# Performance work log

Hardware: AMD Instinct MI355X
Metric: run time of the kernel (lower is better)

## Reference

```python
import jax, jax.numpy as jnp
import numpy as np

N_SRC = 50000
N_DST = 50000
IN_FEATS = 256
OUT_FEATS = 32
NUM_HEADS = 4
N_EDGES = 800000


def setup_inputs() -> dict:
    key = jax.random.key(0)
    ks = jax.random.split(key, 7)
    h_src = jax.random.normal(ks[0], (N_SRC, IN_FEATS), dtype=jnp.float32)
    h_dst = jax.random.normal(ks[1], (N_DST, IN_FEATS), dtype=jnp.float32)
    # xavier-normal-ish scaling for the shared fc weight
    W = jax.random.normal(ks[2], (IN_FEATS, NUM_HEADS * OUT_FEATS), dtype=jnp.float32) * (
        jnp.sqrt(2.0) * jnp.sqrt(2.0 / (IN_FEATS + NUM_HEADS * OUT_FEATS))
    )
    attn_l = jax.random.normal(ks[3], (NUM_HEADS, OUT_FEATS), dtype=jnp.float32) * 0.1
    attn_r = jax.random.normal(ks[4], (NUM_HEADS, OUT_FEATS), dtype=jnp.float32) * 0.1
    src_idx = jax.random.randint(ks[5], (N_EDGES,), 0, N_SRC, dtype=jnp.int32)
    dst_idx = jax.random.randint(ks[6], (N_EDGES,), 0, N_DST, dtype=jnp.int32)
    return {"h_src": h_src, "h_dst": h_dst, "W": W, "attn_l": attn_l,
            "attn_r": attn_r, "src_idx": src_idx, "dst_idx": dst_idx}


def reference(h_src, h_dst, W, attn_l, attn_r, src_idx, dst_idx):
    H, F = NUM_HEADS, OUT_FEATS
    # shared linear projection (no bias), reshape to [N, H, F]
    ft_src = (h_src @ W).reshape(-1, H, F)            # [N_src, H, F]
    ft_dst = (h_dst @ W).reshape(-1, H, F)            # [N_dst, H, F]
    # per-node attention logits, [N, H]
    el = jnp.einsum('nhf,hf->nh', ft_src, attn_l)
    er = jnp.einsum('nhf,hf->nh', ft_dst, attn_r)
    # u_add_v gather over edges, LeakyReLU(0.2) -> [E, H]
    e = jax.nn.leaky_relu(el[src_idx] + er[dst_idx], negative_slope=0.2)
    # edge softmax over incoming edges of each destination node
    smax = jax.ops.segment_max(e, dst_idx, num_segments=N_DST)   # [N_dst, H]
    e_exp = jnp.exp(e - smax[dst_idx])                           # [E, H]
    ssum = jax.ops.segment_sum(e_exp, dst_idx, num_segments=N_DST)
    a = e_exp / ssum[dst_idx]                                    # [E, H]
    # u_mul_e + scatter-sum aggregation -> [N_dst, H, F]
    msg = ft_src[src_idx] * a[:, :, None]
    rst = jax.ops.segment_sum(msg, dst_idx, num_segments=N_DST)
    return rst
```

## Files before the change

### kernel.cpp

```cpp
#include <hip/hip_runtime.h>

#define IN_FEATS 256
#define OUT_FEATS 32
#define NUM_HEADS 4
#define NHF 128

#define NCH 512

typedef __attribute__((ext_vector_type(8))) short short8;
typedef __attribute__((ext_vector_type(4))) float f32x4;

__device__ inline unsigned short f2bf(float f) {
    unsigned int u = __builtin_bit_cast(unsigned int, f);
    u = (u + 0x7fff + ((u >> 16) & 1)) >> 16;
    return (unsigned short)u;
}
__device__ inline float bfhi2f(unsigned int packed_hi) {
    return __builtin_bit_cast(float, packed_hi);
}

__global__ __launch_bounds__(256) void prep_hist(const float* __restrict__ W,
                                                 const float* __restrict__ attn_r,
                                                 const int* __restrict__ dst,
                                                 float* __restrict__ v,
                                                 unsigned short* __restrict__ Wt,
                                                 int* __restrict__ partial,
                                                 int E) {
    const int t = threadIdx.x;
    const int b = blockIdx.x;
    if (b < 128) {
        Wt[b * 256 + t] = f2bf(W[(size_t)t * NHF + b]);
    } else if (b == 128) {
        for (int p = t; p < IN_FEATS * NUM_HEADS; p += 256) {
            int k = p >> 2, h = p & 3;
            const float* wr = W + (size_t)k * NHF + h * OUT_FEATS;
            const float* ar = attn_r + h * OUT_FEATS;
            float s = 0.f;
            #pragma unroll
            for (int f = 0; f < OUT_FEATS; ++f) s += wr[f] * ar[f];
            v[p] = s;
        }
    } else {
        __shared__ int cnt[256];
        const int hb = b - 129;
        const int chunk = (E + NCH - 1) / NCH;
        const int e0 = hb * chunk;
        const int e1 = min(e0 + chunk, E);
        cnt[t] = 0;
        __syncthreads();
        for (int e = e0 + t; e < e1; e += 256)
            atomicAdd(&cnt[dst[e] >> 8], 1);
        __syncthreads();
        partial[hb * 256 + t] = cnt[t];
    }
}

__global__ __launch_bounds__(256) void bin_pairs(const int* __restrict__ src,
                                                 const int* __restrict__ dst,
                                                 const int* __restrict__ partial,
                                                 unsigned int* __restrict__ pairs,
                                                 int* __restrict__ bbase,
                                                 int E) {
    __shared__ int sc[256];
    __shared__ int basel[256];
    __shared__ int cnt[256];
    const int t = threadIdx.x;
    const int b = blockIdx.x;
    const int chunk = (E + NCH - 1) / NCH;
    const int e0 = b * chunk;
    const int e1 = min(e0 + chunk, E);

    int dreg[7], sreg[7];
    #pragma unroll
    for (int i = 0; i < 7; ++i) {
        const int e = e0 + t + i * 256;
        const bool ok = e < e1;
        dreg[i] = ok ? dst[e] : 0;
        sreg[i] = ok ? src[e] : 0;
    }

    int colsum = 0, rowpref = 0;
    {
        int bb = 0;
        #pragma unroll 8
        for (; bb < b; ++bb) {
            const int pv = partial[bb * 256 + t];
            colsum += pv;
            rowpref += pv;
        }
        #pragma unroll 8
        for (; bb < NCH; ++bb) colsum += partial[bb * 256 + t];
    }
    sc[t] = colsum;
    __syncthreads();
    #pragma unroll
    for (int d = 1; d < 256; d <<= 1) {
        int x = (t >= d) ? sc[t - d] : 0;
        __syncthreads();
        sc[t] += x;
        __syncthreads();
    }
    if (b == 0) {
        bbase[t] = sc[t] - colsum;
        if (t == 255) bbase[256] = sc[255];
    }
    basel[t] = (sc[t] - colsum) + rowpref;
    cnt[t] = 0;
    __syncthreads();

    #pragma unroll
    for (int i = 0; i < 7; ++i) {
        const int e = e0 + t + i * 256;
        if (e < e1) {
            const int d = dreg[i];
            const int bk = d >> 8;
            const int o = atomicAdd(&cnt[bk], 1);
            pairs[basel[bk] + o] = (unsigned int)sreg[i] | ((unsigned int)(d & 255) << 16);
        }
    }
    for (int e = e0 + t + 7 * 256; e < e1; e += 256) {
        const int d = dst[e];
        const int bk = d >> 8;
        const int o = atomicAdd(&cnt[bk], 1);
        pairs[basel[bk] + o] = (unsigned int)src[e] | ((unsigned int)(d & 255) << 16);
    }
}

__global__ __launch_bounds__(256) void er_fine(const float* __restrict__ hdst,
                                               const float* __restrict__ v,
                                               float* __restrict__ er, int M,
                                               const unsigned int* __restrict__ pairs,
                                               const int* __restrict__ bbase,
                                               int* __restrict__ off,
                                               int* __restrict__ csr_src,
                                               int nb, int n_dst, int E) {
    __shared__ int cnt[256];
    __shared__ int cur[256];

    if (blockIdx.x < (unsigned)nb) {
        const int t = threadIdx.x;
        const int b = blockIdx.x;
        const int p0 = bbase[b], p1 = bbase[b + 1];
        cnt[t] = 0;
        __syncthreads();
        for (int p = p0 + t; p < p1; p += 256)
            atomicAdd(&cnt[pairs[p] >> 16], 1);
        __syncthreads();
        int vv = cnt[t];
        cur[t] = vv;
        __syncthreads();
        #pragma unroll
        for (int d = 1; d < 256; d <<= 1) {
            int x = (t >= d) ? cur[t - d] : 0;
            __syncthreads();
            cur[t] += x;
            __syncthreads();
        }
        int ex = cur[t] - vv;
        int node = b * 256 + t;
        if (node < n_dst) off[node] = p0 + ex;
        if (b == 0 && t == 0) off[n_dst] = E;
        __syncthreads();
        cur[t] = ex;
        __syncthreads();
        for (int p = p0 + t; p < p1; p += 256) {
            unsigned int pr = pairs[p];
            int o = atomicAdd(&cur[pr >> 16], 1);
            csr_src[p0 + o] = (int)(pr & 0xffffu);
        }
        return;
    }

    int wid  = ((blockIdx.x - nb) * 256 + threadIdx.x) >> 6;
    int lane = threadIdx.x & 63;
    if (wid >= M) return;
    const float4 x = *(const float4*)(hdst + (size_t)wid * IN_FEATS + lane * 4);
    const float4* vp = (const float4*)(v + (size_t)lane * 16);
    float4 v0 = vp[0], v1 = vp[1], v2 = vp[2], v3 = vp[3];
    float a0 = x.x * v0.x + x.y * v1.x + x.z * v2.x + x.w * v3.x;
    float a1 = x.x * v0.y + x.y * v1.y + x.z * v2.y + x.w * v3.y;
    float a2 = x.x * v0.z + x.y * v1.z + x.z * v2.z + x.w * v3.z;
    float a3 = x.x * v0.w + x.y * v1.w + x.z * v2.w + x.w * v3.w;
    #pragma unroll
    for (int m = 32; m >= 1; m >>= 1) {
        a0 += __shfl_xor(a0, m, 64);
        a1 += __shfl_xor(a1, m, 64);
        a2 += __shfl_xor(a2, m, 64);
        a3 += __shfl_xor(a3, m, 64);
    }
    if (lane == 0) *(float4*)(er + (size_t)wid * 4) = make_float4(a0, a1, a2, a3);
}

#define BSTRIDE 136
__global__ __launch_bounds__(256) void gemm_el(const float* __restrict__ A,
                                               const unsigned short* __restrict__ Wt,
                                               const float* __restrict__ attn_l,
                                               unsigned short* __restrict__ ft16,
                                               float* __restrict__ el, int M) {
    __shared__ unsigned short WtL[128 * 256];

    const int wave = threadIdx.x >> 6;
    const int lane = threadIdx.x & 63;
    const int quad = lane >> 4;
    const int mc   = lane & 15;
    const int row_base = blockIdx.x * 64 + wave * 16;

    for (int i = threadIdx.x; i < 4096; i += 256) {
        const int n = i >> 5, c = i & 31;
        const int cs = (c + n) & 31;
        *(uint4*)(WtL + n * 256 + cs * 8) = *(const uint4*)(Wt + n * 256 + c * 8);
    }

    float al[8];
    #pragma unroll
    for (int t = 0; t < 8; ++t) al[t] = attn_l[(t >> 1) * 32 + (t & 1) * 16 + mc];

    const int rowA = min(row_base + mc, M - 1);
    const float* arow = A + (size_t)rowA * IN_FEATS;

    float4 a[8][2];
    #pragma unroll
    for (int kk = 0; kk < 8; ++kk) {
        a[kk][0] = *(const float4*)(arow + kk * 32 + quad * 8);
        a[kk][1] = *(const float4*)(arow + kk * 32 + quad * 8 + 4);
    }

    f32x4 acc[8];
    #pragma unroll
    for (int t = 0; t < 8; ++t) acc[t] = (f32x4){0.f, 0.f, 0.f, 0.f};

    __syncthreads();

    #pragma unroll
    for (int kk = 0; kk < 8; ++kk) {
        short8 af;
        af[0] = (short)f2bf(a[kk][0].x); af[1] = (short)f2bf(a[kk][0].y);
        af[2] = (short)f2bf(a[kk][0].z); af[3] = (short)f2bf(a[kk][0].w);
        af[4] = (short)f2bf(a[kk][1].x); af[5] = (short)f2bf(a[kk][1].y);
        af[6] = (short)f2bf(a[kk][1].z); af[7] = (short)f2bf(a[kk][1].w);
        #pragma unroll
        for (int t = 0; t < 8; ++t) {
            const int n = t * 16 + mc;
            const int c = ((kk << 2) + quad + n) & 31;
            const short8 bf = *(const short8*)(WtL + n * 256 + c * 8);
            acc[t] = __builtin_amdgcn_mfma_f32_16x16x32_bf16(af, bf, acc[t], 0, 0, 0);
        }
    }

    float elp[4][4];
    #pragma unroll
    for (int v = 0; v < 4; ++v)
        #pragma unroll
        for (int h = 0; h < 4; ++h) elp[v][h] = 0.f;
    #pragma unroll
    for (int v = 0; v < 4; ++v)
        #pragma unroll
        for (int t = 0; t < 8; ++t) elp[v][t >> 1] += acc[t][v] * al[t];
    #pragma unroll
    for (int v = 0; v < 4; ++v)
        #pragma unroll
        for (int h = 0; h < 4; ++h) {
            #pragma unroll
            for (int d = 1; d < 16; d <<= 1)
                elp[v][h] += __shfl_xor(elp[v][h], d, 64);
        }

    #pragma unroll
    for (int v = 0; v < 4; ++v) {
        const int rg = row_base + quad * 4 + v;
        if (rg < M && mc < 4) {
            float ev = (mc == 0) ? elp[v][0] : (mc == 1) ? elp[v][1]
                     : (mc == 2) ? elp[v][2] : elp[v][3];
            el[(size_t)rg * 4 + mc] = ev;
        }
    }

    __syncthreads();
    #pragma unroll
    for (int v = 0; v < 4; ++v) {
        const int lr = wave * 16 + quad * 4 + v;
        #pragma unroll
        for (int t = 0; t < 8; ++t)
            WtL[lr * BSTRIDE + t * 16 + mc] = f2bf(acc[t][v]);
    }
    __syncthreads();
    const int rows_in_blk = min(64, M - blockIdx.x * 64);
    for (int i = threadIdx.x; i < 64 * 16; i += 256) {
        const int lr = i >> 4, seg = i & 15;
        if (lr < rows_in_blk)
            *(uint4*)(ft16 + (size_t)(blockIdx.x * 64 + lr) * NHF + seg * 8) =
                *(const uint4*)(WtL + lr * BSTRIDE + seg * 8);
    }
}

__global__ __launch_bounds__(256) void agg_pull(const int* __restrict__ off,
                                                const int* __restrict__ csr_src,
                                                const float* __restrict__ el,
                                                const float* __restrict__ er,
                                                const uint2* __restrict__ ftp,
                                                float* __restrict__ out, int n_dst) {
    const int wid  = (blockIdx.x * blockDim.x + threadIdx.x) >> 6;
    const int lane = threadIdx.x & 63;
    const int half = lane >> 5;
    const int hl   = lane & 31;
    const int node = wid * 2 + half;
    const bool valid = node < n_dst;
    const int nc = valid ? node : 0;
    const int h  = hl >> 3;
    const float er_h = er[nc * 4 + h];
    const int start = off[nc];
    const int end   = valid ? off[nc + 1] : start;
    const int deg   = end - start;
    const int last  = max(end - 1, 0);

    const int sl = csr_src[min(start + hl, last)];

    const int mdeg  = max(deg, __shfl_xor(deg, 32, 64));
    const int iters = (min(mdeg, 32) + 7) >> 3;

    float a0 = 0.f, a1 = 0.f, a2 = 0.f, a3 = 0.f, sw = 0.f;

    float e[8]; uint2 q[8];
    #pragma unroll
    for (int j = 0; j < 8; ++j) {
        const int s = __shfl(sl, j, 32);
        e[j] = el[s * 4 + h];
        q[j] = ftp[s * 32 + hl];
    }

    for (int i = 0; i < iters; ++i) {
        float f[8]; uint2 r[8];
        const int jn = (i + 1) << 3;
        #pragma unroll
        for (int j = 0; j < 8; ++j) {
            const int s = __shfl(sl, min(jn + j, 31), 32);
            f[j] = el[s * 4 + h];
            r[j] = ftp[s * 32 + hl];
        }

        const int kb = start + (i << 3);
        #pragma unroll
        for (int j = 0; j < 8; ++j) {
            float x = e[j] + er_h;
            x = fmaxf(x, 0.2f * x);
            const float w = (kb + j < end) ? __expf(x) : 0.f;
            sw += w;
            a0 = fmaf(bfhi2f(q[j].x << 16),          w, a0);
            a1 = fmaf(bfhi2f(q[j].x & 0xffff0000u),  w, a1);
            a2 = fmaf(bfhi2f(q[j].y << 16),          w, a2);
            a3 = fmaf(bfhi2f(q[j].y & 0xffff0000u),  w, a3);
        }

        #pragma unroll
        for (int j = 0; j < 8; ++j) { e[j] = f[j]; q[j] = r[j]; }
    }

    for (int k = start + 32; k < end; ++k) {
        const int s = csr_src[k];
        float x = el[s * 4 + h] + er_h;
        x = fmaxf(x, 0.2f * x);
        const float w = __expf(x);
        const uint2 qq = ftp[s * 32 + hl];
        sw += w;
        a0 = fmaf(bfhi2f(qq.x << 16),         w, a0);
        a1 = fmaf(bfhi2f(qq.x & 0xffff0000u), w, a1);
        a2 = fmaf(bfhi2f(qq.y << 16),         w, a2);
        a3 = fmaf(bfhi2f(qq.y & 0xffff0000u), w, a3);
    }

    if (valid) {
        const float inv = (deg > 0) ? 1.f / sw : 0.f;
        float4 r;
        r.x = a0 * inv; r.y = a1 * inv; r.z = a2 * inv; r.w = a3 * inv;
        *(float4*)(out + (size_t)node * NHF + hl * 4) = r;
    }
}

extern "C" void kernel_launch(void* const* d_in, const int* in_sizes, int n_in,
                              void* d_out, int out_size, void* d_ws, size_t ws_size,
                              hipStream_t stream) {
    const float* h_src  = (const float*)d_in[0];
    const float* h_dst  = (const float*)d_in[1];
    const float* W      = (const float*)d_in[2];
    const float* attn_l = (const float*)d_in[3];
    const float* attn_r = (const float*)d_in[4];
    const int* src_idx  = (const int*)d_in[5];
    const int* dst_idx  = (const int*)d_in[6];

    const int n_src = in_sizes[0] / IN_FEATS;
    const int n_dst = in_sizes[1] / IN_FEATS;
    const int E     = in_sizes[5];

    const int nb = (n_dst + 255) >> 8;

    char* ws = (char*)d_ws;
    size_t o = 0;
    float* v       = (float*)(ws + o); o += 4096;
    float* el      = (float*)(ws + o); o += (size_t)n_src * 4 * sizeof(float);
    float* er      = (float*)(ws + o); o += (size_t)n_dst * 4 * sizeof(float);
    int*   off     = (int*)(ws + o);   o += ((size_t)n_dst + 16) * sizeof(int);
    int*   bbase   = (int*)(ws + o);   o += 260 * sizeof(int);
    int*   partial = (int*)(ws + o);   o += (size_t)NCH * 256 * sizeof(int);
    unsigned short* Wt = (unsigned short*)(ws + o); o += (size_t)NHF * IN_FEATS * sizeof(unsigned short);
    int*   csr_src = (int*)(ws + o);   o += (size_t)E * sizeof(int);
    unsigned int* pairs = (unsigned int*)(ws + o); o += (size_t)E * sizeof(unsigned int);
    unsigned short* ft16 = (unsigned short*)(ws + o); o += (size_t)n_src * NHF * sizeof(unsigned short);

    float* out = (float*)d_out;

    prep_hist<<<129 + NCH, 256, 0, stream>>>(W, attn_r, dst_idx, v, Wt, partial, E);
    bin_pairs<<<NCH, 256, 0, stream>>>(src_idx, dst_idx, partial, pairs, bbase, E);
    gemm_el<<<(n_src + 63) / 64, 256, 0, stream>>>(h_src, Wt, attn_l, ft16, el, n_src);
    {
        const int er_blocks = (n_dst * 64 + 255) / 256;
        er_fine<<<nb + er_blocks, 256, 0, stream>>>(h_dst, v, er, n_dst, pairs,
                                                    bbase, off, csr_src, nb, n_dst, E);
    }
    {
        const int nwave = (n_dst + 1) >> 1;
        agg_pull<<<(nwave + 3) / 4, 256, 0, stream>>>(off, csr_src, el, er,
                                                      (const uint2*)ft16, out, n_dst);
    }
}
```

Before: 234.9 us.

## Merge edge binning and GEMM into one launch; store CSR sources as 16-bit

The bin_pairs and gemm_el kernels become one launch, with the first NCH blocks doing edge binning and the rest doing the bf16 MFMA projection, so the two independent stages overlap and one launch is saved. CSR source indices are now stored as unsigned short instead of int, halving that array's write and read traffic in er_fine and agg_pull. The binning blocks now reserve the GEMM's 64KB shared buffer, which can lower their occupancy. The 16-bit index depends on n_src fitting in 16 bits, which the existing pair packing already assumed.

```diff
diff --git a/kernel.cpp b/kernel.cpp
--- a/kernel.cpp
+++ b/kernel.cpp
@@ -55,74 +55,179 @@
     }
 }
 
-__global__ __launch_bounds__(256) void bin_pairs(const int* __restrict__ src,
-                                                 const int* __restrict__ dst,
-                                                 const int* __restrict__ partial,
-                                                 unsigned int* __restrict__ pairs,
-                                                 int* __restrict__ bbase,
-                                                 int E) {
-    __shared__ int sc[256];
-    __shared__ int basel[256];
-    __shared__ int cnt[256];
-    const int t = threadIdx.x;
-    const int b = blockIdx.x;
-    const int chunk = (E + NCH - 1) / NCH;
-    const int e0 = b * chunk;
-    const int e1 = min(e0 + chunk, E);
-
-    int dreg[7], sreg[7];
-    #pragma unroll
-    for (int i = 0; i < 7; ++i) {
-        const int e = e0 + t + i * 256;
-        const bool ok = e < e1;
-        dreg[i] = ok ? dst[e] : 0;
-        sreg[i] = ok ? src[e] : 0;
-    }
-
-    int colsum = 0, rowpref = 0;
-    {
-        int bb = 0;
-        #pragma unroll 8
-        for (; bb < b; ++bb) {
-            const int pv = partial[bb * 256 + t];
-            colsum += pv;
-            rowpref += pv;
-        }
-        #pragma unroll 8
-        for (; bb < NCH; ++bb) colsum += partial[bb * 256 + t];
-    }
-    sc[t] = colsum;
-    __syncthreads();
-    #pragma unroll
-    for (int d = 1; d < 256; d <<= 1) {
-        int x = (t >= d) ? sc[t - d] : 0;
-        __syncthreads();
-        sc[t] += x;
-        __syncthreads();
-    }
-    if (b == 0) {
-        bbase[t] = sc[t] - colsum;
-        if (t == 255) bbase[256] = sc[255];
-    }
-    basel[t] = (sc[t] - colsum) + rowpref;
-    cnt[t] = 0;
-    __syncthreads();
-
-    #pragma unroll
-    for (int i = 0; i < 7; ++i) {
-        const int e = e0 + t + i * 256;
-        if (e < e1) {
-            const int d = dreg[i];
+#define BSTRIDE 136
+__global__ __launch_bounds__(256) void bin_gemm(const int* __restrict__ src,
+                                                const int* __restrict__ dst,
+                                                const int* __restrict__ partial,
+                                                unsigned int* __restrict__ pairs,
+                                                int* __restrict__ bbase,
+                                                int E,
+                                                const float* __restrict__ A,
+                                                const unsigned short* __restrict__ Wt,
+                                                const float* __restrict__ attn_l,
+                                                unsigned short* __restrict__ ft16,
+                                                float* __restrict__ el, int M) {
+    __shared__ unsigned short WtL[128 * 256];
+
+    if (blockIdx.x < NCH) {
+        int* sc    = (int*)WtL;
+        int* basel = (int*)WtL + 256;
+        int* cnt   = (int*)WtL + 512;
+        const int t = threadIdx.x;
+        const int b = blockIdx.x;
+        const int chunk = (E + NCH - 1) / NCH;
+        const int e0 = b * chunk;
+        const int e1 = min(e0 + chunk, E);
+
+        int dreg[7], sreg[7];
+        #pragma unroll
+        for (int i = 0; i < 7; ++i) {
+            const int e = e0 + t + i * 256;
+            const bool ok = e < e1;
+            dreg[i] = ok ? dst[e] : 0;
+            sreg[i] = ok ? src[e] : 0;
+        }
+
+        int colsum = 0, rowpref = 0;
+        {
+            int bb = 0;
+            #pragma unroll 8
+            for (; bb < b; ++bb) {
+                const int pv = partial[bb * 256 + t];
+                colsum += pv;
+                rowpref += pv;
+            }
+            #pragma unroll 8
+            for (; bb < NCH; ++bb) colsum += partial[bb * 256 + t];
+        }
+        sc[t] = colsum;
+        __syncthreads();
+        #pragma unroll
+        for (int d = 1; d < 256; d <<= 1) {
+            int x = (t >= d) ? sc[t - d] : 0;
+            __syncthreads();
+            sc[t] += x;
+            __syncthreads();
+        }
+        if (b == 0) {
+            bbase[t] = sc[t] - colsum;
+            if (t == 255) bbase[256] = sc[255];
+        }
+        basel[t] = (sc[t] - colsum) + rowpref;
+        cnt[t] = 0;
+        __syncthreads();
+
+        #pragma unroll
+        for (int i = 0; i < 7; ++i) {
+            const int e = e0 + t + i * 256;
+            if (e < e1) {
+                const int d = dreg[i];
+                const int bk = d >> 8;
+                const int o = atomicAdd(&cnt[bk], 1);
+                pairs[basel[bk] + o] = (unsigned int)sreg[i] | ((unsigned int)(d & 255) << 16);
+            }
+        }
+        for (int e = e0 + t + 7 * 256; e < e1; e += 256) {
+            const int d = dst[e];
             const int bk = d >> 8;
             const int o = atomicAdd(&cnt[bk], 1);
-            pairs[basel[bk] + o] = (unsigned int)sreg[i] | ((unsigned int)(d & 255) << 16);
-        }
-    }
-    for (int e = e0 + t + 7 * 256; e < e1; e += 256) {
-        const int d = dst[e];
-        const int bk = d >> 8;
-        const int o = atomicAdd(&cnt[bk], 1);
-        pairs[basel[bk] + o] = (unsigned int)src[e] | ((unsigned int)(d & 255) << 16);
+            pairs[basel[bk] + o] = (unsigned int)src[e] | ((unsigned int)(d & 255) << 16);
+        }
+        return;
+    }
+
+    const int gb   = blockIdx.x - NCH;
+    const int wave = threadIdx.x >> 6;
+    const int lane = threadIdx.x & 63;
+    const int quad = lane >> 4;
+    const int mc   = lane & 15;
+    const int row_base = gb * 64 + wave * 16;
+
+    for (int i = threadIdx.x; i < 4096; i += 256) {
+        const int n = i >> 5, c = i & 31;
+        const int cs = (c + n) & 31;
+        *(uint4*)(WtL + n * 256 + cs * 8) = *(const uint4*)(Wt + n * 256 + c * 8);
+    }
+
+    float al[8];
+    #pragma unroll
+    for (int t = 0; t < 8; ++t) al[t] = attn_l[(t >> 1) * 32 + (t & 1) * 16 + mc];
+
+    const int rowA = min(row_base + mc, M - 1);
+    const float* arow = A + (size_t)rowA * IN_FEATS;
+
+    float4 a[8][2];
+    #pragma unroll
+    for (int kk = 0; kk < 8; ++kk) {
+        a[kk][0] = *(const float4*)(arow + kk * 32 + quad * 8);
+        a[kk][1] = *(const float4*)(arow + kk * 32 + quad * 8 + 4);
+    }
+
+    f32x4 acc[8];
+    #pragma unroll
+    for (int t = 0; t < 8; ++t) acc[t] = (f32x4){0.f, 0.f, 0.f, 0.f};
+
+    __syncthreads();
+
+    #pragma unroll
+    for (int kk = 0; kk < 8; ++kk) {
+        short8 af;
+        af[0] = (short)f2bf(a[kk][0].x); af[1] = (short)f2bf(a[kk][0].y);
+        af[2] = (short)f2bf(a[kk][0].z); af[3] = (short)f2bf(a[kk][0].w);
+        af[4] = (short)f2bf(a[kk][1].x); af[5] = (short)f2bf(a[kk][1].y);
+        af[6] = (short)f2bf(a[kk][1].z); af[7] = (short)f2bf(a[kk][1].w);
+        #pragma unroll
+        for (int t = 0; t < 8; ++t) {
+            const int n = t * 16 + mc;
+            const int c = ((kk << 2) + quad + n) & 31;
+            const short8 bf = *(const short8*)(WtL + n * 256 + c * 8);
+            acc[t] = __builtin_amdgcn_mfma_f32_16x16x32_bf16(af, bf, acc[t], 0, 0, 0);
+        }
+    }
+
+    float elp[4][4];
+    #pragma unroll
+    for (int v = 0; v < 4; ++v)
+        #pragma unroll
+        for (int h = 0; h < 4; ++h) elp[v][h] = 0.f;
+    #pragma unroll
+    for (int v = 0; v < 4; ++v)
+        #pragma unroll
+        for (int t = 0; t < 8; ++t) elp[v][t >> 1] += acc[t][v] * al[t];
+    #pragma unroll
+    for (int v = 0; v < 4; ++v)
+        #pragma unroll
+        for (int h = 0; h < 4; ++h) {
+            #pragma unroll
+            for (int d = 1; d < 16; d <<= 1)
+                elp[v][h] += __shfl_xor(elp[v][h], d, 64);
+        }
+
+    #pragma unroll
+    for (int v = 0; v < 4; ++v) {
+        const int rg = row_base + quad * 4 + v;
+        if (rg < M && mc < 4) {
+            float ev = (mc == 0) ? elp[v][0] : (mc == 1) ? elp[v][1]
+                     : (mc == 2) ? elp[v][2] : elp[v][3];
+            el[(size_t)rg * 4 + mc] = ev;
+        }
+    }
+
+    __syncthreads();
+    #pragma unroll
+    for (int v = 0; v < 4; ++v) {
+        const int lr = wave * 16 + quad * 4 + v;
+        #pragma unroll
+        for (int t = 0; t < 8; ++t)
+            WtL[lr * BSTRIDE + t * 16 + mc] = f2bf(acc[t][v]);
+    }
+    __syncthreads();
+    const int rows_in_blk = min(64, M - gb * 64);
+    for (int i = threadIdx.x; i < 64 * 16; i += 256) {
+        const int lr = i >> 4, seg = i & 15;
+        if (lr < rows_in_blk)
+            *(uint4*)(ft16 + (size_t)(gb * 64 + lr) * NHF + seg * 8) =
+                *(const uint4*)(WtL + lr * BSTRIDE + seg * 8);
     }
 }
 
@@ -132,7 +237,7 @@
                                                const unsigned int* __restrict__ pairs,
                                                const int* __restrict__ bbase,
                                                int* __restrict__ off,
-                                               int* __restrict__ csr_src,
+                                               unsigned short* __restrict__ csr16,
                                                int nb, int n_dst, int E) {
     __shared__ int cnt[256];
     __shared__ int cur[256];
@@ -166,7 +271,7 @@
         for (int p = p0 + t; p < p1; p += 256) {
             unsigned int pr = pairs[p];
             int o = atomicAdd(&cur[pr >> 16], 1);
-            csr_src[p0 + o] = (int)(pr & 0xffffu);
+            csr16[p0 + o] = (unsigned short)(pr & 0xffffu);
         }
         return;
     }
@@ -191,110 +296,8 @@
     if (lane == 0) *(float4*)(er + (size_t)wid * 4) = make_float4(a0, a1, a2, a3);
 }
 
-#define BSTRIDE 136
-__global__ __launch_bounds__(256) void gemm_el(const float* __restrict__ A,
-                                               const unsigned short* __restrict__ Wt,
-                                               const float* __restrict__ attn_l,
-                                               unsigned short* __restrict__ ft16,
-                                               float* __restrict__ el, int M) {
-    __shared__ unsigned short WtL[128 * 256];
-
-    const int wave = threadIdx.x >> 6;
-    const int lane = threadIdx.x & 63;
-    const int quad = lane >> 4;
-    const int mc   = lane & 15;
-    const int row_base = blockIdx.x * 64 + wave * 16;
-
-    for (int i = threadIdx.x; i < 4096; i += 256) {
-        const int n = i >> 5, c = i & 31;
-        const int cs = (c + n) & 31;
-        *(uint4*)(WtL + n * 256 + cs * 8) = *(const uint4*)(Wt + n * 256 + c * 8);
-    }
-
-    float al[8];
-    #pragma unroll
-    for (int t = 0; t < 8; ++t) al[t] = attn_l[(t >> 1) * 32 + (t & 1) * 16 + mc];
-
-    const int rowA = min(row_base + mc, M - 1);
-    const float* arow = A + (size_t)rowA * IN_FEATS;
-
-    float4 a[8][2];
-    #pragma unroll
-    for (int kk = 0; kk < 8; ++kk) {
-        a[kk][0] = *(const float4*)(arow + kk * 32 + quad * 8);
-        a[kk][1] = *(const float4*)(arow + kk * 32 + quad * 8 + 4);
-    }
-
-    f32x4 acc[8];
-    #pragma unroll
-    for (int t = 0; t < 8; ++t) acc[t] = (f32x4){0.f, 0.f, 0.f, 0.f};
-
-    __syncthreads();
-
-    #pragma unroll
-    for (int kk = 0; kk < 8; ++kk) {
-        short8 af;
-        af[0] = (short)f2bf(a[kk][0].x); af[1] = (short)f2bf(a[kk][0].y);
-        af[2] = (short)f2bf(a[kk][0].z); af[3] = (short)f2bf(a[kk][0].w);
-        af[4] = (short)f2bf(a[kk][1].x); af[5] = (short)f2bf(a[kk][1].y);
-        af[6] = (short)f2bf(a[kk][1].z); af[7] = (short)f2bf(a[kk][1].w);
-        #pragma unroll
-        for (int t = 0; t < 8; ++t) {
-            const int n = t * 16 + mc;
-            const int c = ((kk << 2) + quad + n) & 31;
-            const short8 bf = *(const short8*)(WtL + n * 256 + c * 8);
-            acc[t] = __builtin_amdgcn_mfma_f32_16x16x32_bf16(af, bf, acc[t], 0, 0, 0);
-        }
-    }
-
-    float elp[4][4];
-    #pragma unroll
-    for (int v = 0; v < 4; ++v)
-        #pragma unroll
-        for (int h = 0; h < 4; ++h) elp[v][h] = 0.f;
-    #pragma unroll
-    for (int v = 0; v < 4; ++v)
-        #pragma unroll
-        for (int t = 0; t < 8; ++t) elp[v][t >> 1] += acc[t][v] * al[t];
-    #pragma unroll
-    for (int v = 0; v < 4; ++v)
-        #pragma unroll
-        for (int h = 0; h < 4; ++h) {
-            #pragma unroll
-            for (int d = 1; d < 16; d <<= 1)
-                elp[v][h] += __shfl_xor(elp[v][h], d, 64);
-        }
-
-    #pragma unroll
-    for (int v = 0; v < 4; ++v) {
-        const int rg = row_base + quad * 4 + v;
-        if (rg < M && mc < 4) {
-            float ev = (mc == 0) ? elp[v][0] : (mc == 1) ? elp[v][1]
-                     : (mc == 2) ? elp[v][2] : elp[v][3];
-            el[(size_t)rg * 4 + mc] = ev;
-        }
-    }
-
-    __syncthreads();
-    #pragma unroll
-    for (int v = 0; v < 4; ++v) {
-        const int lr = wave * 16 + quad * 4 + v;
-        #pragma unroll
-        for (int t = 0; t < 8; ++t)
-            WtL[lr * BSTRIDE + t * 16 + mc] = f2bf(acc[t][v]);
-    }
-    __syncthreads();
-    const int rows_in_blk = min(64, M - blockIdx.x * 64);
-    for (int i = threadIdx.x; i < 64 * 16; i += 256) {
-        const int lr = i >> 4, seg = i & 15;
-        if (lr < rows_in_blk)
-            *(uint4*)(ft16 + (size_t)(blockIdx.x * 64 + lr) * NHF + seg * 8) =
-                *(const uint4*)(WtL + lr * BSTRIDE + seg * 8);
-    }
-}
-
 __global__ __launch_bounds__(256) void agg_pull(const int* __restrict__ off,
-                                                const int* __restrict__ csr_src,
+                                                const unsigned short* __restrict__ csr16,
                                                 const float* __restrict__ el,
                                                 const float* __restrict__ er,
                                                 const uint2* __restrict__ ftp,
@@ -313,7 +316,7 @@
     const int deg   = end - start;
     const int last  = max(end - 1, 0);
 
-    const int sl = csr_src[min(start + hl, last)];
+    const int sl = (int)csr16[min(start + hl, last)];
 
     const int mdeg  = max(deg, __shfl_xor(deg, 32, 64));
     const int iters = (min(mdeg, 32) + 7) >> 3;
@@ -356,7 +359,7 @@
     }
 
     for (int k = start + 32; k < end; ++k) {
-        const int s = csr_src[k];
+        const int s = (int)csr16[k];
         float x = el[s * 4 + h] + er_h;
         x = fmaxf(x, 0.2f * x);
         const float w = __expf(x);
@@ -402,23 +405,24 @@
     int*   bbase   = (int*)(ws + o);   o += 260 * sizeof(int);
     int*   partial = (int*)(ws + o);   o += (size_t)NCH * 256 * sizeof(int);
     unsigned short* Wt = (unsigned short*)(ws + o); o += (size_t)NHF * IN_FEATS * sizeof(unsigned short);
-    int*   csr_src = (int*)(ws + o);   o += (size_t)E * sizeof(int);
+    unsigned short* csr16 = (unsigned short*)(ws + o); o += (((size_t)E * 2 + 15) & ~15ull);
     unsigned int* pairs = (unsigned int*)(ws + o); o += (size_t)E * sizeof(unsigned int);
     unsigned short* ft16 = (unsigned short*)(ws + o); o += (size_t)n_src * NHF * sizeof(unsigned short);
 
     float* out = (float*)d_out;
 
     prep_hist<<<129 + NCH, 256, 0, stream>>>(W, attn_r, dst_idx, v, Wt, partial, E);
-    bin_pairs<<<NCH, 256, 0, stream>>>(src_idx, dst_idx, partial, pairs, bbase, E);
-    gemm_el<<<(n_src + 63) / 64, 256, 0, stream>>>(h_src, Wt, attn_l, ft16, el, n_src);
+    bin_gemm<<<NCH + (n_src + 63) / 64, 256, 0, stream>>>(src_idx, dst_idx, partial,
+                                                          pairs, bbase, E,
+                                                          h_src, Wt, attn_l, ft16, el, n_src);
     {
         const int er_blocks = (n_dst * 64 + 255) / 256;
         er_fine<<<nb + er_blocks, 256, 0, stream>>>(h_dst, v, er, n_dst, pairs,
-                                                    bbase, off, csr_src, nb, n_dst, E);
+                                                    bbase, off, csr16, nb, n_dst, E);
     }
     {
         const int nwave = (n_dst + 1) >> 1;
-        agg_pull<<<(nwave + 3) / 4, 256, 0, stream>>>(off, csr_src, el, er,
+        agg_pull<<<(nwave + 3) / 4, 256, 0, stream>>>(off, csr16, el, er,
                                                       (const uint2*)ft16, out, n_dst);
     }
 }
```

Result: no change. 231.7 us (-1.4%).
